# Kernel optimization log

Measured on AMD Instinct MI355X. Metric: run time of the kernel, lower is better.

Reference implementation:

```python
import jax, jax.numpy as jnp
import numpy as np
from jax import lax

DT = 0.01
DT_SCALE = 1.0


def setup_inputs() -> dict:
    key = jax.random.key(0)
    ks = jax.random.split(key, 5)
    B, D, R = 32768, 256, 32
    return {
        "x": jax.random.normal(ks[0], (B, D), dtype=jnp.float32),
        "v": jax.random.normal(ks[1], (B, D), dtype=jnp.float32),
        "force": jax.random.normal(ks[2], (B, D), dtype=jnp.float32),
        "U": jax.random.normal(ks[3], (D, R), dtype=jnp.float32) * 0.1,
        "W": jax.random.normal(ks[4], (R, D), dtype=jnp.float32) * 0.1,
        "steps": 8,
    }


def reference(x, v, force, U, W, steps):
    # Low-rank quadratic-form christoffel: gamma(v) = ((v @ U)**2) @ W.
    # Friction mu = 0.0 (christoffel returns a single tensor in the original).
    eff_dt = DT * DT_SCALE
    h = 0.5 * eff_dt
    mu = 0.0

    def christoffel(vv):
        return jnp.einsum("br,rd->bd", jnp.einsum("bd,dr->br", vv, U) ** 2, W)

    def step(carry, _):
        cx, cv = carry
        gamma = christoffel(cv)
        v_half = (cv + h * (force - gamma)) / (1.0 + h * mu)
        cx = cx + eff_dt * v_half
        # topology 0 -> Euclidean boundary: identity
        gamma_half = christoffel(v_half)
        cv = (v_half + h * (force - gamma_half)) / (1.0 + h * mu)
        return (cx, cv), None

    (cx, cv), _ = lax.scan(step, (x, v), None, length=steps)
    return cx, cv
```

## Files before the change

kernel.cpp:

```cpp
#include <hip/hip_runtime.h>

typedef __attribute__((ext_vector_type(4))) float f32x4;
typedef __attribute__((ext_vector_type(8))) short bf16x8;

constexpr float EFF_DT = 0.01f;
constexpr float HH     = 0.005f;
constexpr float INV_DT = 100.0f;

__device__ inline short f2bf(float x){
    union{float f;unsigned u;}c; c.f=x;
    unsigned r=c.u+0x7FFFu+((c.u>>16)&1u);
    return (short)(r>>16);
}
__device__ inline unsigned cvtpk(float lo,float hi){
    unsigned r; asm("v_cvt_pk_bf16_f32 %0, %1, %2":"=v"(r):"v"(lo),"v"(hi)); return r;
}
__device__ inline float ubflo(unsigned u){union{unsigned x;float f;}c;c.x=u<<16;return c.f;}
__device__ inline float ubfhi(unsigned u){union{unsigned x;float f;}c;c.x=u&0xffff0000u;return c.f;}

union VP4 { unsigned u[4]; bf16x8 h; };

__global__ __launch_bounds__(256,2) void leapfrog_v8(
    const float* __restrict__ x_in, const float* __restrict__ v_in,
    const float* __restrict__ f_in, const float* __restrict__ Ug,
    const float* __restrict__ Wg, const int* __restrict__ steps_p,
    float* __restrict__ out)
{
    __shared__ __align__(16) char lds[81920];
    short* WF = (short*)lds;

    const int tid=threadIdx.x, w=tid>>6, lane=tid&63, g=lane>>4, c=lane&15;
    const int R0 = blockIdx.x*64 + w*16;
    const int gb = (R0+c)*256 + g*4;
    const int BD = 32768*256;
    float* xw = (float*)(lds + 16384 + w*16384);

    f32x4 vv[16];
    unsigned fpk[16][2];
    bf16x8 uf[2][8];

    #pragma unroll
    for(int dt=0;dt<16;++dt) vv[dt] = *(const f32x4*)&v_in[gb+dt*16];

    #pragma unroll
    for(int rt=0;rt<2;++rt){
        #pragma unroll
        for(int cc=0;cc<8;++cc){
            bf16x8 e;
            #pragma unroll
            for(int j=0;j<8;++j){
                const int kk = ((j>>2)<<4) + g*4 + (j&3);
                e[j] = f2bf(Ug[(cc*32+kk)*32 + rt*16 + c]);
            }
            uf[rt][cc] = e;
        }
    }
    #pragma unroll
    for(int i=0;i<4;++i){
        const int t = w*4+i;
        bf16x8 e;
        #pragma unroll
        for(int j=0;j<8;++j){
            const int kk = ((j>>2)<<4) + g*4 + (j&3);
            e[j] = f2bf(HH * Wg[kk*256 + t*16 + c]);
        }
        *(bf16x8*)&WF[t*512 + lane*8] = e;
    }
    #pragma unroll
    for(int dt=0;dt<16;++dt){
        f32x4 ff = *(const f32x4*)&f_in[gb+dt*16];
        fpk[dt][0]=cvtpk(HH*ff[0],HH*ff[1]);
        fpk[dt][1]=cvtpk(HH*ff[2],HH*ff[3]);
    }
    #pragma unroll
    for(int dt=0;dt<16;++dt){
        f32x4 xx = *(const f32x4*)&x_in[gb+dt*16];
        f32x4 xs; xs[0]=INV_DT*xx[0]; xs[1]=INV_DT*xx[1];
        xs[2]=INV_DT*xx[2]; xs[3]=INV_DT*xx[3];
        *(f32x4*)&xw[dt*256 + lane*4] = xs;
    }
    __syncthreads();

    const int nsteps = *steps_p;
    const f32x4 zero = {0.f,0.f,0.f,0.f};

#define PHASE_AB(ACCX, STX, STV) do { \
    f32x4 a00=zero,a01=zero,a10=zero,a11=zero; \
    _Pragma("unroll") \
    for(int cc=0;cc<8;++cc){ \
        VP4 vp; \
        vp.u[0]=cvtpk(vv[2*cc][0],  vv[2*cc][1]); \
        vp.u[1]=cvtpk(vv[2*cc][2],  vv[2*cc][3]); \
        vp.u[2]=cvtpk(vv[2*cc+1][0],vv[2*cc+1][1]); \
        vp.u[3]=cvtpk(vv[2*cc+1][2],vv[2*cc+1][3]); \
        if(cc&1){ a01=__builtin_amdgcn_mfma_f32_16x16x32_bf16(uf[0][cc],vp.h,a01,0,0,0); \
                  a11=__builtin_amdgcn_mfma_f32_16x16x32_bf16(uf[1][cc],vp.h,a11,0,0,0); } \
        else    { a00=__builtin_amdgcn_mfma_f32_16x16x32_bf16(uf[0][cc],vp.h,a00,0,0,0); \
                  a10=__builtin_amdgcn_mfma_f32_16x16x32_bf16(uf[1][cc],vp.h,a10,0,0,0); } \
    } \
    { \
        float t00=a00[0]+a01[0], t01=a00[1]+a01[1], t02=a00[2]+a01[2], t03=a00[3]+a01[3]; \
        float t10=a10[0]+a11[0], t11=a10[1]+a11[1], t12=a10[2]+a11[2], t13=a10[3]+a11[3]; \
        VP4 t2; \
        t2.u[0]=cvtpk(t00*t00, t01*t01); \
        t2.u[1]=cvtpk(t02*t02, t03*t03); \
        t2.u[2]=cvtpk(t10*t10, t11*t11); \
        t2.u[3]=cvtpk(t12*t12, t13*t13); \
        _Pragma("unroll") \
        for(int dt=0;dt<16;++dt){ \
            bf16x8 wf=*(bf16x8*)&WF[dt*512 + lane*8]; \
            f32x4 gm=__builtin_amdgcn_mfma_f32_16x16x32_bf16(wf,t2.h,zero,0,0,0); \
            const unsigned f0=fpk[dt][0], f1=fpk[dt][1]; \
            f32x4 nv; \
            nv[0]=(vv[dt][0]+ubflo(f0))-gm[0]; \
            nv[1]=(vv[dt][1]+ubfhi(f0))-gm[1]; \
            nv[2]=(vv[dt][2]+ubflo(f1))-gm[2]; \
            nv[3]=(vv[dt][3]+ubfhi(f1))-gm[3]; \
            vv[dt]=nv; \
            if(ACCX){ \
                f32x4* xp=(f32x4*)&xw[dt*256 + lane*4]; \
                f32x4 xv=*xp; \
                xv[0]+=nv[0]; xv[1]+=nv[1]; xv[2]+=nv[2]; xv[3]+=nv[3]; \
                if(STX){ \
                    f32x4 xo; \
                    xo[0]=EFF_DT*xv[0]; xo[1]=EFF_DT*xv[1]; \
                    xo[2]=EFF_DT*xv[2]; xo[3]=EFF_DT*xv[3]; \
                    *(f32x4*)&out[gb+dt*16] = xo; \
                }else{ \
                    *xp = xv; \
                } \
            } \
            if(STV){ \
                *(f32x4*)&out[BD+gb+dt*16] = nv; \
            } \
        } \
    } \
} while(0)

    for(int s=0;s<nsteps-1;++s){
        PHASE_AB(1,0,0);
        PHASE_AB(0,0,0);
    }
    PHASE_AB(1,1,0);
    PHASE_AB(0,0,1);
#undef PHASE_AB
}

extern "C" void kernel_launch(void* const* d_in, const int* in_sizes, int n_in,
                              void* d_out, int out_size, void* d_ws, size_t ws_size,
                              hipStream_t stream) {
    (void)in_sizes; (void)n_in; (void)d_ws; (void)ws_size; (void)out_size;
    const float* x_in = (const float*)d_in[0];
    const float* v_in = (const float*)d_in[1];
    const float* f_in = (const float*)d_in[2];
    const float* Ug   = (const float*)d_in[3];
    const float* Wg   = (const float*)d_in[4];
    const int*   st   = (const int*)d_in[5];
    float* out = (float*)d_out;

    dim3 grid(32768/64), block(256);
    hipLaunchKernelGGL(leapfrog_v8, grid, block, 0, stream,
                       x_in, v_in, f_in, Ug, Wg, st, out);
}
```

Before: 48.56 us.

## Split each 16-row tile's D dimension across two waves with LDS reduction

Each 16-row tile is now handled by two waves that each own half of the 256 feature columns, replacing the old scheme of one wave per 16 rows. The rank-32 projection is computed as partial sums, exchanged through LDS, and completed after a block barrier. The x accumulator moves from LDS into registers using fma, which removes the LDS read-modify-write per element. The change halves per-thread register state so more blocks fit per CU (launch bounds 128,3) and grows the grid to 2048 blocks, at the cost of two __syncthreads and extra LDS traffic per phase.

```diff
diff --git a/kernel.cpp b/kernel.cpp
--- a/kernel.cpp
+++ b/kernel.cpp
@@ -5,7 +5,6 @@
 
 constexpr float EFF_DT = 0.01f;
 constexpr float HH     = 0.005f;
-constexpr float INV_DT = 100.0f;
 
 __device__ inline short f2bf(float x){
     union{float f;unsigned u;}c; c.f=x;
@@ -20,44 +19,47 @@
 
 union VP4 { unsigned u[4]; bf16x8 h; };
 
-__global__ __launch_bounds__(256,2) void leapfrog_v8(
+__global__ __launch_bounds__(128,3) void leapfrog_v9(
     const float* __restrict__ x_in, const float* __restrict__ v_in,
     const float* __restrict__ f_in, const float* __restrict__ Ug,
     const float* __restrict__ Wg, const int* __restrict__ steps_p,
     float* __restrict__ out)
 {
-    __shared__ __align__(16) char lds[81920];
-    short* WF = (short*)lds;
+    __shared__ __align__(16) char lds[32768];
+    short* WF  = (short*)lds;
+    f32x4* TEX = (f32x4*)(lds + 16384);
 
-    const int tid=threadIdx.x, w=tid>>6, lane=tid&63, g=lane>>4, c=lane&15;
-    const int R0 = blockIdx.x*64 + w*16;
+    const int tid=threadIdx.x, dh=tid>>6, lane=tid&63, g=lane>>4, c=lane&15;
+    const int R0 = blockIdx.x*16;
     const int gb = (R0+c)*256 + g*4;
     const int BD = 32768*256;
-    float* xw = (float*)(lds + 16384 + w*16384);
+    const int db = dh*8;
 
-    f32x4 vv[16];
-    unsigned fpk[16][2];
-    bf16x8 uf[2][8];
+    f32x4 vv[8], xacc[8];
+    unsigned fpk[8][2];
+    bf16x8 uf[2][4];
 
     #pragma unroll
-    for(int dt=0;dt<16;++dt) vv[dt] = *(const f32x4*)&v_in[gb+dt*16];
+    for(int i=0;i<8;++i) vv[i] = *(const f32x4*)&v_in[gb + (db+i)*16];
+    #pragma unroll
+    for(int i=0;i<8;++i) xacc[i] = *(const f32x4*)&x_in[gb + (db+i)*16];
 
     #pragma unroll
     for(int rt=0;rt<2;++rt){
         #pragma unroll
-        for(int cc=0;cc<8;++cc){
+        for(int cq=0;cq<4;++cq){
             bf16x8 e;
             #pragma unroll
             for(int j=0;j<8;++j){
                 const int kk = ((j>>2)<<4) + g*4 + (j&3);
-                e[j] = f2bf(Ug[(cc*32+kk)*32 + rt*16 + c]);
+                e[j] = f2bf(Ug[((dh*4+cq)*32+kk)*32 + rt*16 + c]);
             }
-            uf[rt][cc] = e;
+            uf[rt][cq] = e;
         }
     }
     #pragma unroll
-    for(int i=0;i<4;++i){
-        const int t = w*4+i;
+    for(int i=0;i<8;++i){
+        const int t = db + i;
         bf16x8 e;
         #pragma unroll
         for(int j=0;j<8;++j){
@@ -67,83 +69,75 @@
         *(bf16x8*)&WF[t*512 + lane*8] = e;
     }
     #pragma unroll
-    for(int dt=0;dt<16;++dt){
-        f32x4 ff = *(const f32x4*)&f_in[gb+dt*16];
-        fpk[dt][0]=cvtpk(HH*ff[0],HH*ff[1]);
-        fpk[dt][1]=cvtpk(HH*ff[2],HH*ff[3]);
+    for(int i=0;i<8;++i){
+        f32x4 ff = *(const f32x4*)&f_in[gb + (db+i)*16];
+        fpk[i][0]=cvtpk(HH*ff[0],HH*ff[1]);
+        fpk[i][1]=cvtpk(HH*ff[2],HH*ff[3]);
     }
-    #pragma unroll
-    for(int dt=0;dt<16;++dt){
-        f32x4 xx = *(const f32x4*)&x_in[gb+dt*16];
-        f32x4 xs; xs[0]=INV_DT*xx[0]; xs[1]=INV_DT*xx[1];
-        xs[2]=INV_DT*xx[2]; xs[3]=INV_DT*xx[3];
-        *(f32x4*)&xw[dt*256 + lane*4] = xs;
-    }
-    __syncthreads();
 
     const int nsteps = *steps_p;
     const f32x4 zero = {0.f,0.f,0.f,0.f};
 
-#define PHASE_AB(ACCX, STX, STV) do { \
+#define PH(HALF, ACCX, STX, STV) do{ \
     f32x4 a00=zero,a01=zero,a10=zero,a11=zero; \
     _Pragma("unroll") \
-    for(int cc=0;cc<8;++cc){ \
+    for(int cq=0;cq<4;++cq){ \
         VP4 vp; \
-        vp.u[0]=cvtpk(vv[2*cc][0],  vv[2*cc][1]); \
-        vp.u[1]=cvtpk(vv[2*cc][2],  vv[2*cc][3]); \
-        vp.u[2]=cvtpk(vv[2*cc+1][0],vv[2*cc+1][1]); \
-        vp.u[3]=cvtpk(vv[2*cc+1][2],vv[2*cc+1][3]); \
-        if(cc&1){ a01=__builtin_amdgcn_mfma_f32_16x16x32_bf16(uf[0][cc],vp.h,a01,0,0,0); \
-                  a11=__builtin_amdgcn_mfma_f32_16x16x32_bf16(uf[1][cc],vp.h,a11,0,0,0); } \
-        else    { a00=__builtin_amdgcn_mfma_f32_16x16x32_bf16(uf[0][cc],vp.h,a00,0,0,0); \
-                  a10=__builtin_amdgcn_mfma_f32_16x16x32_bf16(uf[1][cc],vp.h,a10,0,0,0); } \
+        vp.u[0]=cvtpk(vv[2*cq][0],  vv[2*cq][1]); \
+        vp.u[1]=cvtpk(vv[2*cq][2],  vv[2*cq][3]); \
+        vp.u[2]=cvtpk(vv[2*cq+1][0],vv[2*cq+1][1]); \
+        vp.u[3]=cvtpk(vv[2*cq+1][2],vv[2*cq+1][3]); \
+        if(cq&1){ a01=__builtin_amdgcn_mfma_f32_16x16x32_bf16(uf[0][cq],vp.h,a01,0,0,0); \
+                  a11=__builtin_amdgcn_mfma_f32_16x16x32_bf16(uf[1][cq],vp.h,a11,0,0,0); } \
+        else    { a00=__builtin_amdgcn_mfma_f32_16x16x32_bf16(uf[0][cq],vp.h,a00,0,0,0); \
+                  a10=__builtin_amdgcn_mfma_f32_16x16x32_bf16(uf[1][cq],vp.h,a10,0,0,0); } \
     } \
+    f32x4 p0, p1; \
+    p0[0]=a00[0]+a01[0]; p0[1]=a00[1]+a01[1]; p0[2]=a00[2]+a01[2]; p0[3]=a00[3]+a01[3]; \
+    p1[0]=a10[0]+a11[0]; p1[1]=a10[1]+a11[1]; p1[2]=a10[2]+a11[2]; p1[3]=a10[3]+a11[3]; \
+    TEX[(((HALF)*2+dh)*2+0)*64+lane]=p0; \
+    TEX[(((HALF)*2+dh)*2+1)*64+lane]=p1; \
+    __syncthreads(); \
     { \
-        float t00=a00[0]+a01[0], t01=a00[1]+a01[1], t02=a00[2]+a01[2], t03=a00[3]+a01[3]; \
-        float t10=a10[0]+a11[0], t11=a10[1]+a11[1], t12=a10[2]+a11[2], t13=a10[3]+a11[3]; \
+        f32x4 q0=TEX[(((HALF)*2+(1-dh))*2+0)*64+lane]; \
+        f32x4 q1=TEX[(((HALF)*2+(1-dh))*2+1)*64+lane]; \
+        float s0=p0[0]+q0[0], s1=p0[1]+q0[1], s2=p0[2]+q0[2], s3=p0[3]+q0[3]; \
+        float s4=p1[0]+q1[0], s5=p1[1]+q1[1], s6=p1[2]+q1[2], s7=p1[3]+q1[3]; \
         VP4 t2; \
-        t2.u[0]=cvtpk(t00*t00, t01*t01); \
-        t2.u[1]=cvtpk(t02*t02, t03*t03); \
-        t2.u[2]=cvtpk(t10*t10, t11*t11); \
-        t2.u[3]=cvtpk(t12*t12, t13*t13); \
+        t2.u[0]=cvtpk(s0*s0, s1*s1); \
+        t2.u[1]=cvtpk(s2*s2, s3*s3); \
+        t2.u[2]=cvtpk(s4*s4, s5*s5); \
+        t2.u[3]=cvtpk(s6*s6, s7*s7); \
         _Pragma("unroll") \
-        for(int dt=0;dt<16;++dt){ \
-            bf16x8 wf=*(bf16x8*)&WF[dt*512 + lane*8]; \
+        for(int i=0;i<8;++i){ \
+            bf16x8 wf=*(bf16x8*)&WF[(db+i)*512 + lane*8]; \
             f32x4 gm=__builtin_amdgcn_mfma_f32_16x16x32_bf16(wf,t2.h,zero,0,0,0); \
-            const unsigned f0=fpk[dt][0], f1=fpk[dt][1]; \
+            const unsigned f0=fpk[i][0], f1=fpk[i][1]; \
             f32x4 nv; \
-            nv[0]=(vv[dt][0]+ubflo(f0))-gm[0]; \
-            nv[1]=(vv[dt][1]+ubfhi(f0))-gm[1]; \
-            nv[2]=(vv[dt][2]+ubflo(f1))-gm[2]; \
-            nv[3]=(vv[dt][3]+ubfhi(f1))-gm[3]; \
-            vv[dt]=nv; \
+            nv[0]=(vv[i][0]+ubflo(f0))-gm[0]; \
+            nv[1]=(vv[i][1]+ubfhi(f0))-gm[1]; \
+            nv[2]=(vv[i][2]+ubflo(f1))-gm[2]; \
+            nv[3]=(vv[i][3]+ubfhi(f1))-gm[3]; \
+            vv[i]=nv; \
             if(ACCX){ \
-                f32x4* xp=(f32x4*)&xw[dt*256 + lane*4]; \
-                f32x4 xv=*xp; \
-                xv[0]+=nv[0]; xv[1]+=nv[1]; xv[2]+=nv[2]; xv[3]+=nv[3]; \
-                if(STX){ \
-                    f32x4 xo; \
-                    xo[0]=EFF_DT*xv[0]; xo[1]=EFF_DT*xv[1]; \
-                    xo[2]=EFF_DT*xv[2]; xo[3]=EFF_DT*xv[3]; \
-                    *(f32x4*)&out[gb+dt*16] = xo; \
-                }else{ \
-                    *xp = xv; \
-                } \
+                xacc[i][0]=fmaf(EFF_DT,nv[0],xacc[i][0]); \
+                xacc[i][1]=fmaf(EFF_DT,nv[1],xacc[i][1]); \
+                xacc[i][2]=fmaf(EFF_DT,nv[2],xacc[i][2]); \
+                xacc[i][3]=fmaf(EFF_DT,nv[3],xacc[i][3]); \
+                if(STX){ *(f32x4*)&out[gb+(db+i)*16] = xacc[i]; } \
             } \
-            if(STV){ \
-                *(f32x4*)&out[BD+gb+dt*16] = nv; \
-            } \
+            if(STV){ *(f32x4*)&out[BD+gb+(db+i)*16] = nv; } \
         } \
     } \
-} while(0)
+}while(0)
 
     for(int s=0;s<nsteps-1;++s){
-        PHASE_AB(1,0,0);
-        PHASE_AB(0,0,0);
+        PH(0, 1,0,0);
+        PH(1, 0,0,0);
     }
-    PHASE_AB(1,1,0);
-    PHASE_AB(0,0,1);
-#undef PHASE_AB
+    PH(0, 1,1,0);
+    PH(1, 0,0,1);
+#undef PH
 }
 
 extern "C" void kernel_launch(void* const* d_in, const int* in_sizes, int n_in,
@@ -158,7 +152,7 @@
     const int*   st   = (const int*)d_in[5];
     float* out = (float*)d_out;
 
-    dim3 grid(32768/64), block(256);
-    hipLaunchKernelGGL(leapfrog_v8, grid, block, 0, stream,
+    dim3 grid(32768/16), block(128);
+    hipLaunchKernelGGL(leapfrog_v9, grid, block, 0, stream,
                        x_in, v_in, f_in, Ug, Wg, st, out);
 }
```

Measured after the change: 63.56 us. +30.9%, slower.
